# Optimization experiments

Hardware: AMD Instinct MI355X
Metric: run time of the kernel (lower is better)

## Reference

```python
import jax, jax.numpy as jnp
import numpy as np

D_MODEL = 1024
N_HEADS = 16
D_K = D_MODEL // N_HEADS
BATCH = 2
SEQ = 2048


def setup_inputs() -> dict:
    key = jax.random.key(0)
    ks = jax.random.split(key, 9)
    s = 1.0 / np.sqrt(D_MODEL)
    x = jax.random.normal(ks[0], (BATCH, SEQ, D_MODEL), dtype=jnp.float32)
    # nn.Linear params: weight [out, in], bias [out]
    w_q = jax.random.uniform(ks[1], (D_MODEL, D_MODEL), jnp.float32, -s, s)
    b_q = jax.random.uniform(ks[2], (D_MODEL,), jnp.float32, -s, s)
    w_k = jax.random.uniform(ks[3], (D_MODEL, D_MODEL), jnp.float32, -s, s)
    b_k = jax.random.uniform(ks[4], (D_MODEL,), jnp.float32, -s, s)
    w_v = jax.random.uniform(ks[5], (D_MODEL, D_MODEL), jnp.float32, -s, s)
    b_v = jax.random.uniform(ks[6], (D_MODEL,), jnp.float32, -s, s)
    w_o = jax.random.uniform(ks[7], (D_MODEL, D_MODEL), jnp.float32, -s, s)
    b_o = jax.random.uniform(ks[8], (D_MODEL,), jnp.float32, -s, s)
    return {"x": x, "w_q": w_q, "b_q": b_q, "w_k": w_k, "b_k": b_k,
            "w_v": w_v, "b_v": b_v, "w_o": w_o, "b_o": b_o}


def reference(x, w_q, b_q, w_k, b_k, w_v, b_v, w_o, b_o):
    B, S, _ = x.shape
    # Linear projections, then split heads: [B, H, S, d_k]
    def proj(w, b):
        y = jnp.einsum('bsd,ed->bse', x, w) + b
        return y.reshape(B, S, N_HEADS, D_K).transpose(0, 2, 1, 3)
    q = proj(w_q, b_q)
    k = proj(w_k, b_k)
    v = proj(w_v, b_v)
    scores = jnp.einsum('bhqd,bhkd->bhqk', q, k) / jnp.sqrt(jnp.float32(D_K))
    attn = jax.nn.softmax(scores, axis=-1)  # dropout is identity in eval mode
    out = jnp.einsum('bhqk,bhkd->bhqd', attn, v)
    out = out.transpose(0, 2, 1, 3).reshape(B, S, D_MODEL)
    out = jnp.einsum('bsd,ed->bse', out, w_o) + b_o
    return out, attn
```

## Files before the change

### kernel.cpp

```cpp
#include <hip/hip_runtime.h>
#include <hip/hip_bf16.h>
#include <stdint.h>


typedef __attribute__((ext_vector_type(4))) float f32x4;
typedef __attribute__((ext_vector_type(8))) short s16x8;
typedef __attribute__((ext_vector_type(4))) unsigned short u16x4;

#define MFMA(a, b, c) __builtin_amdgcn_mfma_f32_16x16x32_bf16((a), (b), (c), 0, 0, 0)

__device__ __forceinline__ unsigned short f2bf(float f) {
    unsigned int u = __float_as_uint(f);
    unsigned int r = (u + 0x7FFFu + ((u >> 16) & 1u)) >> 16;
    return (unsigned short)r;
}

__global__ void convert_kernel(const float* __restrict__ x,
                               const float* __restrict__ wq, const float* __restrict__ wk,
                               const float* __restrict__ wv, const float* __restrict__ wo,
                               unsigned short* __restrict__ xb, unsigned short* __restrict__ wb) {
    size_t g = (size_t)blockIdx.x * blockDim.x + threadIdx.x;
    size_t i4 = g * 4;
    const float* src;
    unsigned short* dst;
    size_t off;
    if (i4 < 4194304) {
        src = x; dst = xb; off = i4;
    } else {
        size_t j = i4 - 4194304;
        int wsel = (int)(j >> 20);
        off = j & 1048575;
        src = (wsel == 0) ? wq : (wsel == 1) ? wk : (wsel == 2) ? wv : wo;
        dst = wb + ((size_t)wsel << 20);
    }
    float4 v = *(const float4*)(src + off);
    u16x4 o;
    o[0] = f2bf(v.x); o[1] = f2bf(v.y); o[2] = f2bf(v.z); o[3] = f2bf(v.w);
    *(u16x4*)(dst + off) = o;
}

__global__ __launch_bounds__(256, 2) void gemm_kernel(
    const unsigned short* __restrict__ A, const unsigned short* __restrict__ B,
    const float* __restrict__ bias_q, const float* __restrict__ bias_k,
    const float* __restrict__ bias_v, int mode,
    unsigned short* __restrict__ Qs, unsigned short* __restrict__ Kb,
    unsigned short* __restrict__ Vt, float* __restrict__ outp) {
    const int t = threadIdx.x;
    const int lane = t & 63;
    const int w = t >> 6;
    const int wr = w >> 1, wc = w & 1;
    const int rowbase = blockIdx.y * 128;
    const int colbase = blockIdx.x * 128;

    __shared__ unsigned short lA[2][128 * 40];
    __shared__ unsigned short lB[2][128 * 40];

    const int sr = t >> 2;
    const int sc = (t & 3) * 8;

    const unsigned short* gA0 = A + (size_t)(rowbase + sr) * 1024 + sc;
    const unsigned short* gA1 = A + (size_t)(rowbase + sr + 64) * 1024 + sc;
    const unsigned short* gB0 = B + (size_t)(colbase + sr) * 1024 + sc;
    const unsigned short* gB1 = B + (size_t)(colbase + sr + 64) * 1024 + sc;

    f32x4 acc[4][4];
#pragma unroll
    for (int mi = 0; mi < 4; ++mi)
#pragma unroll
        for (int ni = 0; ni < 4; ++ni)
            acc[mi][ni] = (f32x4){0.f, 0.f, 0.f, 0.f};

    uint4 va0 = *(const uint4*)(gA0);
    uint4 va1 = *(const uint4*)(gA1);
    uint4 vb0 = *(const uint4*)(gB0);
    uint4 vb1 = *(const uint4*)(gB1);
    *(uint4*)&lA[0][sr * 40 + sc] = va0;
    *(uint4*)&lA[0][(sr + 64) * 40 + sc] = va1;
    *(uint4*)&lB[0][sr * 40 + sc] = vb0;
    *(uint4*)&lB[0][(sr + 64) * 40 + sc] = vb1;
    __syncthreads();

    const int koff = (lane >> 4) * 8;
    const int ar = wr * 64 + (lane & 15);
    const int br = wc * 64 + (lane & 15);

    int cur = 0;
    for (int kt = 0; kt < 32; ++kt) {
        if (kt < 31) {
            int ko = (kt + 1) * 32;
            va0 = *(const uint4*)(gA0 + ko);
            va1 = *(const uint4*)(gA1 + ko);
            vb0 = *(const uint4*)(gB0 + ko);
            vb1 = *(const uint4*)(gB1 + ko);
        }
        s16x8 af[4], bf[4];
#pragma unroll
        for (int mi = 0; mi < 4; ++mi)
            af[mi] = *(const s16x8*)&lA[cur][(ar + mi * 16) * 40 + koff];
#pragma unroll
        for (int ni = 0; ni < 4; ++ni)
            bf[ni] = *(const s16x8*)&lB[cur][(br + ni * 16) * 40 + koff];
#pragma unroll
        for (int mi = 0; mi < 4; ++mi)
#pragma unroll
            for (int ni = 0; ni < 4; ++ni)
                acc[mi][ni] = MFMA(af[mi], bf[ni], acc[mi][ni]);
        if (kt < 31) {
            int nb = cur ^ 1;
            *(uint4*)&lA[nb][sr * 40 + sc] = va0;
            *(uint4*)&lA[nb][(sr + 64) * 40 + sc] = va1;
            *(uint4*)&lB[nb][sr * 40 + sc] = vb0;
            *(uint4*)&lB[nb][(sr + 64) * 40 + sc] = vb1;
        }
        __syncthreads();
        cur ^= 1;
    }

    if (mode == 1) {
#pragma unroll
        for (int ni = 0; ni < 4; ++ni) {
            int n = colbase + wc * 64 + ni * 16 + (lane & 15);
            float bv = bias_q[n];
#pragma unroll
            for (int mi = 0; mi < 4; ++mi) {
#pragma unroll
                for (int reg = 0; reg < 4; ++reg) {
                    int m = rowbase + wr * 64 + mi * 16 + (lane >> 4) * 4 + reg;
                    outp[(size_t)m * 1024 + n] = acc[mi][ni][reg] + bv;
                }
            }
        }
    } else {
        const int proj = colbase >> 10;
        const float* bias = (proj == 0) ? bias_q : (proj == 1) ? bias_k : bias_v;
        const float scale = (proj == 0) ? 0.18033688011112042f : 1.0f;
#pragma unroll
        for (int ni = 0; ni < 4; ++ni) {
            int n = colbase + wc * 64 + ni * 16 + (lane & 15);
            int nn = n & 1023;
            int h = nn >> 6, d = nn & 63;
            float bv = bias[nn];
#pragma unroll
            for (int mi = 0; mi < 4; ++mi) {
                int m0 = rowbase + wr * 64 + mi * 16 + (lane >> 4) * 4;
                int b = m0 >> 11, s0 = m0 & 2047;
                if (proj == 2) {
                    u16x4 pk;
#pragma unroll
                    for (int reg = 0; reg < 4; ++reg)
                        pk[reg] = f2bf(acc[mi][ni][reg] + bv);
                    *(u16x4*)&Vt[((size_t)(b * 16 + h) * 64 + d) * 2048 + s0] = pk;
                } else {
                    unsigned short* dstp = (proj == 0) ? Qs : Kb;
#pragma unroll
                    for (int reg = 0; reg < 4; ++reg)
                        dstp[((size_t)(b * 16 + h) * 2048 + (s0 + reg)) * 64 + d] =
                            f2bf((acc[mi][ni][reg] + bv) * scale);
                }
            }
        }
    }
}

__global__ __launch_bounds__(256, 2) void attn_kernel(
    const unsigned short* __restrict__ Qs, const unsigned short* __restrict__ Kb,
    const unsigned short* __restrict__ Vt, float* __restrict__ attn,
    unsigned short* __restrict__ ctx) {
    const int t = threadIdx.x;
    const int lane = t & 63;
    const int w = t >> 6;
    const int wr = w >> 1, wc = w & 1;
    const int qt = blockIdx.x;
    const int bh = blockIdx.y;
    const int b = bh >> 4, h = bh & 15;

    const unsigned short* Qh = Qs + (size_t)bh * (2048 * 64);
    const unsigned short* Kh = Kb + (size_t)bh * (2048 * 64);
    const unsigned short* Vh = Vt + (size_t)bh * (64 * 2048);
    float* attn_h = attn + (size_t)bh * (2048 * 2048) + (size_t)qt * (128 * 2048);

    __shared__ unsigned short lQ[128 * 72];
    __shared__ unsigned short lK[64 * 72];
    __shared__ unsigned short lV[64 * 72];
    __shared__ unsigned short lP[128 * 72];
    __shared__ float lred[2][128];

    const int sr8 = t >> 3;
    const int sc8 = (t & 7) * 8;

    {
#pragma unroll
        for (int rr = 0; rr < 4; ++rr) {
            uint4 v = *(const uint4*)&Qh[((size_t)(qt * 128 + sr8 + rr * 32)) * 64 + sc8];
            *(uint4*)&lQ[(sr8 + rr * 32) * 72 + sc8] = v;
        }
    }

    const int koff = (lane >> 4) * 8;
    const int ar = wr * 64 + (lane & 15);
    const int brc = wc * 32 + (lane & 15);

    float lsum[4][4];
#pragma unroll
    for (int mi = 0; mi < 4; ++mi)
#pragma unroll
        for (int reg = 0; reg < 4; ++reg) lsum[mi][reg] = 0.f;

    for (int kt = 0; kt < 32; ++kt) {
        __syncthreads();
        uint4 kv0 = *(const uint4*)&Kh[((size_t)(kt * 64 + sr8)) * 64 + sc8];
        uint4 kv1 = *(const uint4*)&Kh[((size_t)(kt * 64 + sr8 + 32)) * 64 + sc8];
        *(uint4*)&lK[sr8 * 72 + sc8] = kv0;
        *(uint4*)&lK[(sr8 + 32) * 72 + sc8] = kv1;
        __syncthreads();
        f32x4 sacc[4][2];
#pragma unroll
        for (int mi = 0; mi < 4; ++mi)
#pragma unroll
            for (int ni = 0; ni < 2; ++ni) sacc[mi][ni] = (f32x4){0.f, 0.f, 0.f, 0.f};
#pragma unroll
        for (int kk = 0; kk < 2; ++kk) {
            s16x8 qf[4], kf[2];
#pragma unroll
            for (int mi = 0; mi < 4; ++mi)
                qf[mi] = *(const s16x8*)&lQ[(ar + mi * 16) * 72 + kk * 32 + koff];
#pragma unroll
            for (int ni = 0; ni < 2; ++ni)
                kf[ni] = *(const s16x8*)&lK[(brc + ni * 16) * 72 + kk * 32 + koff];
#pragma unroll
            for (int mi = 0; mi < 4; ++mi)
#pragma unroll
                for (int ni = 0; ni < 2; ++ni)
                    sacc[mi][ni] = MFMA(qf[mi], kf[ni], sacc[mi][ni]);
        }
#pragma unroll
        for (int mi = 0; mi < 4; ++mi) {
#pragma unroll
            for (int reg = 0; reg < 4; ++reg) {
                float e = exp2f(sacc[mi][0][reg]) + exp2f(sacc[mi][1][reg]);
                e += __shfl_xor(e, 1);
                e += __shfl_xor(e, 2);
                e += __shfl_xor(e, 4);
                e += __shfl_xor(e, 8);
                lsum[mi][reg] += e;
            }
        }
    }
    if ((lane & 15) == 0) {
#pragma unroll
        for (int mi = 0; mi < 4; ++mi)
#pragma unroll
            for (int reg = 0; reg < 4; ++reg)
                lred[wc][wr * 64 + mi * 16 + (lane >> 4) * 4 + reg] = lsum[mi][reg];
    }
    __syncthreads();
    float rl[4][4];
#pragma unroll
    for (int mi = 0; mi < 4; ++mi)
#pragma unroll
        for (int reg = 0; reg < 4; ++reg) {
            int row = wr * 64 + mi * 16 + (lane >> 4) * 4 + reg;
            rl[mi][reg] = 1.0f / (lred[0][row] + lred[1][row]);
        }

    f32x4 oacc[4][2];
#pragma unroll
    for (int mi = 0; mi < 4; ++mi)
#pragma unroll
        for (int ni = 0; ni < 2; ++ni) oacc[mi][ni] = (f32x4){0.f, 0.f, 0.f, 0.f};

    for (int kt = 0; kt < 32; ++kt) {
        __syncthreads();
        uint4 kv0 = *(const uint4*)&Kh[((size_t)(kt * 64 + sr8)) * 64 + sc8];
        uint4 kv1 = *(const uint4*)&Kh[((size_t)(kt * 64 + sr8 + 32)) * 64 + sc8];
        uint4 vv0 = *(const uint4*)&Vh[(size_t)sr8 * 2048 + kt * 64 + sc8];
        uint4 vv1 = *(const uint4*)&Vh[(size_t)(sr8 + 32) * 2048 + kt * 64 + sc8];
        *(uint4*)&lK[sr8 * 72 + sc8] = kv0;
        *(uint4*)&lK[(sr8 + 32) * 72 + sc8] = kv1;
        *(uint4*)&lV[sr8 * 72 + sc8] = vv0;
        *(uint4*)&lV[(sr8 + 32) * 72 + sc8] = vv1;
        __syncthreads();
        f32x4 sacc[4][2];
#pragma unroll
        for (int mi = 0; mi < 4; ++mi)
#pragma unroll
            for (int ni = 0; ni < 2; ++ni) sacc[mi][ni] = (f32x4){0.f, 0.f, 0.f, 0.f};
#pragma unroll
        for (int kk = 0; kk < 2; ++kk) {
            s16x8 qf[4], kf[2];
#pragma unroll
            for (int mi = 0; mi < 4; ++mi)
                qf[mi] = *(const s16x8*)&lQ[(ar + mi * 16) * 72 + kk * 32 + koff];
#pragma unroll
            for (int ni = 0; ni < 2; ++ni)
                kf[ni] = *(const s16x8*)&lK[(brc + ni * 16) * 72 + kk * 32 + koff];
#pragma unroll
            for (int mi = 0; mi < 4; ++mi)
#pragma unroll
                for (int ni = 0; ni < 2; ++ni)
                    sacc[mi][ni] = MFMA(qf[mi], kf[ni], sacc[mi][ni]);
        }
#pragma unroll
        for (int mi = 0; mi < 4; ++mi) {
#pragma unroll
            for (int ni = 0; ni < 2; ++ni) {
                int coll = wc * 32 + ni * 16 + (lane & 15);
                int colg = kt * 64 + coll;
#pragma unroll
                for (int reg = 0; reg < 4; ++reg) {
                    int row = wr * 64 + mi * 16 + (lane >> 4) * 4 + reg;
                    float p = exp2f(sacc[mi][ni][reg]) * rl[mi][reg];
                    attn_h[(size_t)row * 2048 + colg] = p;
                    lP[row * 72 + coll] = f2bf(p);
                }
            }
        }
        __syncthreads();
#pragma unroll
        for (int ks = 0; ks < 2; ++ks) {
            s16x8 pf[4], vf[2];
#pragma unroll
            for (int mi = 0; mi < 4; ++mi)
                pf[mi] = *(const s16x8*)&lP[(ar + mi * 16) * 72 + ks * 32 + koff];
#pragma unroll
            for (int ni = 0; ni < 2; ++ni)
                vf[ni] = *(const s16x8*)&lV[(brc + ni * 16) * 72 + ks * 32 + koff];
#pragma unroll
            for (int mi = 0; mi < 4; ++mi)
#pragma unroll
                for (int ni = 0; ni < 2; ++ni)
                    oacc[mi][ni] = MFMA(pf[mi], vf[ni], oacc[mi][ni]);
        }
    }

#pragma unroll
    for (int mi = 0; mi < 4; ++mi) {
#pragma unroll
        for (int ni = 0; ni < 2; ++ni) {
            int d = wc * 32 + ni * 16 + (lane & 15);
#pragma unroll
            for (int reg = 0; reg < 4; ++reg) {
                int q = qt * 128 + wr * 64 + mi * 16 + (lane >> 4) * 4 + reg;
                ctx[((size_t)(b * 2048 + q)) * 1024 + h * 64 + d] = f2bf(oacc[mi][ni][reg]);
            }
        }
    }
}

extern "C" void kernel_launch(void* const* d_in, const int* in_sizes, int n_in,
                              void* d_out, int out_size, void* d_ws, size_t ws_size,
                              hipStream_t stream) {
    const float* x  = (const float*)d_in[0];
    const float* wq = (const float*)d_in[1];
    const float* bq = (const float*)d_in[2];
    const float* wk = (const float*)d_in[3];
    const float* bk = (const float*)d_in[4];
    const float* wv = (const float*)d_in[5];
    const float* bv = (const float*)d_in[6];
    const float* wo = (const float*)d_in[7];
    const float* bo = (const float*)d_in[8];

    char* ws = (char*)d_ws;
    unsigned short* xb  = (unsigned short*)(ws);
    unsigned short* wb  = (unsigned short*)(ws + 8388608);
    unsigned short* Qsc = (unsigned short*)(ws + 16777216);
    unsigned short* Kb  = (unsigned short*)(ws + 25165824);
    unsigned short* Vt  = (unsigned short*)(ws + 33554432);
    unsigned short* ctx = (unsigned short*)(ws + 41943040);

    float* out  = (float*)d_out;
    float* attn = out + 4194304;

    convert_kernel<<<8192, 256, 0, stream>>>(x, wq, wk, wv, wo, xb, wb);
    gemm_kernel<<<dim3(24, 32), 256, 0, stream>>>(xb, wb, bq, bk, bv, 0,
                                                  Qsc, Kb, Vt, nullptr);
    attn_kernel<<<dim3(16, 32), 256, 0, stream>>>(Qsc, Kb, Vt, attn, ctx);
    gemm_kernel<<<dim3(8, 32), 256, 0, stream>>>(ctx, wb + 3 * 1048576, bo, bo, bo, 1,
                                                 nullptr, nullptr, nullptr, out);
}
```

Baseline: 312.4 us.

## Load attention Q/K/V fragments directly into registers and prefetch next tile

After: 277.4 us. 1.13x faster.

```diff
diff --git a/kernel.cpp b/kernel.cpp
--- a/kernel.cpp
+++ b/kernel.cpp
@@ -168,6 +168,9 @@
     unsigned short* __restrict__ ctx) {
     const int t = threadIdx.x;
     const int lane = t & 63;
+    const int l15 = lane & 15;
+    const int g = lane >> 4;
+    const int g4 = g * 4, g8 = g * 8;
     const int w = t >> 6;
     const int wr = w >> 1, wc = w & 1;
     const int qt = blockIdx.x;
@@ -177,174 +180,157 @@
     const unsigned short* Qh = Qs + (size_t)bh * (2048 * 64);
     const unsigned short* Kh = Kb + (size_t)bh * (2048 * 64);
     const unsigned short* Vh = Vt + (size_t)bh * (64 * 2048);
-    float* attn_h = attn + (size_t)bh * (2048 * 2048) + (size_t)qt * (128 * 2048);
-
-    __shared__ unsigned short lQ[128 * 72];
-    __shared__ unsigned short lK[64 * 72];
-    __shared__ unsigned short lV[64 * 72];
-    __shared__ unsigned short lP[128 * 72];
+    float* attn_h = attn + (size_t)bh * (2048 * 2048) + (size_t)(qt * 128) * 2048;
+
+    __shared__ unsigned short lP[2][128 * 72];
     __shared__ float lred[2][128];
 
-    const int sr8 = t >> 3;
-    const int sc8 = (t & 7) * 8;
-
-    {
-#pragma unroll
-        for (int rr = 0; rr < 4; ++rr) {
-            uint4 v = *(const uint4*)&Qh[((size_t)(qt * 128 + sr8 + rr * 32)) * 64 + sc8];
-            *(uint4*)&lQ[(sr8 + rr * 32) * 72 + sc8] = v;
-        }
-    }
-
-    const int koff = (lane >> 4) * 8;
-    const int ar = wr * 64 + (lane & 15);
-    const int brc = wc * 32 + (lane & 15);
-
-    float lsum[4][4];
+    s16x8 qf[8];
 #pragma unroll
     for (int mi = 0; mi < 4; ++mi)
 #pragma unroll
-        for (int reg = 0; reg < 4; ++reg) lsum[mi][reg] = 0.f;
-
-    for (int kt = 0; kt < 32; ++kt) {
-        __syncthreads();
-        uint4 kv0 = *(const uint4*)&Kh[((size_t)(kt * 64 + sr8)) * 64 + sc8];
-        uint4 kv1 = *(const uint4*)&Kh[((size_t)(kt * 64 + sr8 + 32)) * 64 + sc8];
-        *(uint4*)&lK[sr8 * 72 + sc8] = kv0;
-        *(uint4*)&lK[(sr8 + 32) * 72 + sc8] = kv1;
-        __syncthreads();
-        f32x4 sacc[4][2];
+        for (int kk = 0; kk < 2; ++kk)
+            qf[mi * 2 + kk] =
+                *(const s16x8*)&Qh[(size_t)(qt * 128 + wr * 64 + mi * 16 + l15) * 64 + kk * 32 + g8];
+
+    s16x8 kf0[4], kf1[4], vf0[4], vf1[4];
+
+#define K_LOAD(DST, KT)                                                                     \
+    {                                                                                       \
+        _Pragma("unroll") for (int ni = 0; ni < 2; ++ni)                                    \
+            _Pragma("unroll") for (int kk = 0; kk < 2; ++kk)                                \
+                DST[ni * 2 + kk] = *(const s16x8*)&Kh[(size_t)((KT) * 64 + wc * 32 +        \
+                                                               ni * 16 + l15) * 64 +        \
+                                                      kk * 32 + g8];                        \
+    }
+#define V_LOAD(DST, KT)                                                                     \
+    {                                                                                       \
+        _Pragma("unroll") for (int ni = 0; ni < 2; ++ni)                                    \
+            _Pragma("unroll") for (int ks = 0; ks < 2; ++ks)                                \
+                DST[ni * 2 + ks] = *(const s16x8*)&Vh[(size_t)(wc * 32 + ni * 16 + l15) *   \
+                                                          2048 +                            \
+                                                      (KT) * 64 + ks * 32 + g8];            \
+    }
+#define QK_MFMA(KF, SACC)                                                                   \
+    {                                                                                       \
+        _Pragma("unroll") for (int kk = 0; kk < 2; ++kk)                                    \
+            _Pragma("unroll") for (int mi = 0; mi < 4; ++mi)                                \
+                _Pragma("unroll") for (int ni = 0; ni < 2; ++ni)                            \
+                    SACC[mi][ni] = MFMA(KF[ni * 2 + kk], qf[mi * 2 + kk], SACC[mi][ni]);    \
+    }
+
+    float qsum[4] = {0.f, 0.f, 0.f, 0.f};
+    K_LOAD(kf0, 0);
+#define P1_BODY(KF, KFN, KT)                                                                \
+    {                                                                                       \
+        f32x4 sacc[4][2];                                                                   \
+        _Pragma("unroll") for (int mi = 0; mi < 4; ++mi)                                    \
+            _Pragma("unroll") for (int ni = 0; ni < 2; ++ni)                                \
+                sacc[mi][ni] = (f32x4){0.f, 0.f, 0.f, 0.f};                                 \
+        QK_MFMA(KF, sacc);                                                                  \
+        if ((KT) < 31) K_LOAD(KFN, (KT) + 1);                                               \
+        _Pragma("unroll") for (int mi = 0; mi < 4; ++mi) {                                  \
+            float e = 0.f;                                                                  \
+            _Pragma("unroll") for (int ni = 0; ni < 2; ++ni)                                \
+                _Pragma("unroll") for (int r = 0; r < 4; ++r)                               \
+                    e += exp2f(sacc[mi][ni][r]);                                            \
+            qsum[mi] += e;                                                                  \
+        }                                                                                   \
+    }
+    for (int k2 = 0; k2 < 16; ++k2) {
+        P1_BODY(kf0, kf1, 2 * k2);
+        P1_BODY(kf1, kf0, 2 * k2 + 1);
+    }
+#pragma unroll
+    for (int mi = 0; mi < 4; ++mi) {
+        float v = qsum[mi];
+        v += __shfl_xor(v, 16);
+        v += __shfl_xor(v, 32);
+        qsum[mi] = v;
+    }
+    if (lane < 16) {
 #pragma unroll
         for (int mi = 0; mi < 4; ++mi)
-#pragma unroll
-            for (int ni = 0; ni < 2; ++ni) sacc[mi][ni] = (f32x4){0.f, 0.f, 0.f, 0.f};
-#pragma unroll
-        for (int kk = 0; kk < 2; ++kk) {
-            s16x8 qf[4], kf[2];
-#pragma unroll
-            for (int mi = 0; mi < 4; ++mi)
-                qf[mi] = *(const s16x8*)&lQ[(ar + mi * 16) * 72 + kk * 32 + koff];
-#pragma unroll
-            for (int ni = 0; ni < 2; ++ni)
-                kf[ni] = *(const s16x8*)&lK[(brc + ni * 16) * 72 + kk * 32 + koff];
-#pragma unroll
-            for (int mi = 0; mi < 4; ++mi)
-#pragma unroll
-                for (int ni = 0; ni < 2; ++ni)
-                    sacc[mi][ni] = MFMA(qf[mi], kf[ni], sacc[mi][ni]);
-        }
-#pragma unroll
-        for (int mi = 0; mi < 4; ++mi) {
-#pragma unroll
-            for (int reg = 0; reg < 4; ++reg) {
-                float e = exp2f(sacc[mi][0][reg]) + exp2f(sacc[mi][1][reg]);
-                e += __shfl_xor(e, 1);
-                e += __shfl_xor(e, 2);
-                e += __shfl_xor(e, 4);
-                e += __shfl_xor(e, 8);
-                lsum[mi][reg] += e;
+            lred[wc][wr * 64 + mi * 16 + lane] = qsum[mi];
+    }
+    __syncthreads();
+    float rl[4];
+#pragma unroll
+    for (int mi = 0; mi < 4; ++mi) {
+        int q = wr * 64 + mi * 16 + l15;
+        rl[mi] = 1.0f / (lred[0][q] + lred[1][q]);
+    }
+
+    f32x4 oacc[4][2];
+#pragma unroll
+    for (int mi = 0; mi < 4; ++mi)
+#pragma unroll
+        for (int ni = 0; ni < 2; ++ni) oacc[mi][ni] = (f32x4){0.f, 0.f, 0.f, 0.f};
+
+    K_LOAD(kf0, 0);
+    V_LOAD(vf0, 0);
+#define P2_BODY(BUF, KF, KFN, VF, VFN, KT)                                                  \
+    {                                                                                       \
+        f32x4 sacc[4][2];                                                                   \
+        _Pragma("unroll") for (int mi = 0; mi < 4; ++mi)                                    \
+            _Pragma("unroll") for (int ni = 0; ni < 2; ++ni)                                \
+                sacc[mi][ni] = (f32x4){0.f, 0.f, 0.f, 0.f};                                 \
+        QK_MFMA(KF, sacc);                                                                  \
+        if ((KT) < 31) {                                                                    \
+            K_LOAD(KFN, (KT) + 1);                                                          \
+            V_LOAD(VFN, (KT) + 1);                                                          \
+        }                                                                                   \
+        _Pragma("unroll") for (int mi = 0; mi < 4; ++mi) {                                  \
+            const int q = wr * 64 + mi * 16 + l15;                                          \
+            _Pragma("unroll") for (int ni = 0; ni < 2; ++ni) {                              \
+                float4 pv;                                                                  \
+                pv.x = exp2f(sacc[mi][ni][0]) * rl[mi];                                     \
+                pv.y = exp2f(sacc[mi][ni][1]) * rl[mi];                                     \
+                pv.z = exp2f(sacc[mi][ni][2]) * rl[mi];                                     \
+                pv.w = exp2f(sacc[mi][ni][3]) * rl[mi];                                     \
+                *(float4*)&attn_h[(size_t)q * 2048 + (KT) * 64 + wc * 32 + ni * 16 + g4] =  \
+                    pv;                                                                     \
+                u16x4 pk;                                                                   \
+                pk[0] = f2bf(pv.x);                                                         \
+                pk[1] = f2bf(pv.y);                                                         \
+                pk[2] = f2bf(pv.z);                                                         \
+                pk[3] = f2bf(pv.w);                                                         \
+                *(u16x4*)&lP[BUF][q * 72 + wc * 32 + ni * 16 + g4] = pk;                    \
+            }                                                                               \
+        }                                                                                   \
+        __syncthreads();                                                                    \
+        _Pragma("unroll") for (int ks = 0; ks < 2; ++ks) {                                  \
+            s16x8 pf[4];                                                                    \
+            _Pragma("unroll") for (int mi = 0; mi < 4; ++mi)                                \
+                pf[mi] =                                                                    \
+                    *(const s16x8*)&lP[BUF][(wr * 64 + mi * 16 + l15) * 72 + ks * 32 + g8]; \
+            _Pragma("unroll") for (int mi = 0; mi < 4; ++mi)                                \
+                _Pragma("unroll") for (int ni = 0; ni < 2; ++ni)                            \
+                    oacc[mi][ni] = MFMA(pf[mi], VF[ni * 2 + ks], oacc[mi][ni]);             \
+        }                                                                                   \
+    }
+    for (int k2 = 0; k2 < 16; ++k2) {
+        P2_BODY(0, kf0, kf1, vf0, vf1, 2 * k2);
+        P2_BODY(1, kf1, kf0, vf1, vf0, 2 * k2 + 1);
+    }
+
+#pragma unroll
+    for (int mi = 0; mi < 4; ++mi) {
+#pragma unroll
+        for (int ni = 0; ni < 2; ++ni) {
+            int d = wc * 32 + ni * 16 + l15;
+#pragma unroll
+            for (int r = 0; r < 4; ++r) {
+                int q = qt * 128 + wr * 64 + mi * 16 + g4 + r;
+                ctx[((size_t)(b * 2048 + q)) * 1024 + h * 64 + d] = f2bf(oacc[mi][ni][r]);
             }
         }
     }
-    if ((lane & 15) == 0) {
-#pragma unroll
-        for (int mi = 0; mi < 4; ++mi)
-#pragma unroll
-            for (int reg = 0; reg < 4; ++reg)
-                lred[wc][wr * 64 + mi * 16 + (lane >> 4) * 4 + reg] = lsum[mi][reg];
-    }
-    __syncthreads();
-    float rl[4][4];
-#pragma unroll
-    for (int mi = 0; mi < 4; ++mi)
-#pragma unroll
-        for (int reg = 0; reg < 4; ++reg) {
-            int row = wr * 64 + mi * 16 + (lane >> 4) * 4 + reg;
-            rl[mi][reg] = 1.0f / (lred[0][row] + lred[1][row]);
-        }
-
-    f32x4 oacc[4][2];
-#pragma unroll
-    for (int mi = 0; mi < 4; ++mi)
-#pragma unroll
-        for (int ni = 0; ni < 2; ++ni) oacc[mi][ni] = (f32x4){0.f, 0.f, 0.f, 0.f};
-
-    for (int kt = 0; kt < 32; ++kt) {
-        __syncthreads();
-        uint4 kv0 = *(const uint4*)&Kh[((size_t)(kt * 64 + sr8)) * 64 + sc8];
-        uint4 kv1 = *(const uint4*)&Kh[((size_t)(kt * 64 + sr8 + 32)) * 64 + sc8];
-        uint4 vv0 = *(const uint4*)&Vh[(size_t)sr8 * 2048 + kt * 64 + sc8];
-        uint4 vv1 = *(const uint4*)&Vh[(size_t)(sr8 + 32) * 2048 + kt * 64 + sc8];
-        *(uint4*)&lK[sr8 * 72 + sc8] = kv0;
-        *(uint4*)&lK[(sr8 + 32) * 72 + sc8] = kv1;
-        *(uint4*)&lV[sr8 * 72 + sc8] = vv0;
-        *(uint4*)&lV[(sr8 + 32) * 72 + sc8] = vv1;
-        __syncthreads();
-        f32x4 sacc[4][2];
-#pragma unroll
-        for (int mi = 0; mi < 4; ++mi)
-#pragma unroll
-            for (int ni = 0; ni < 2; ++ni) sacc[mi][ni] = (f32x4){0.f, 0.f, 0.f, 0.f};
-#pragma unroll
-        for (int kk = 0; kk < 2; ++kk) {
-            s16x8 qf[4], kf[2];
-#pragma unroll
-            for (int mi = 0; mi < 4; ++mi)
-                qf[mi] = *(const s16x8*)&lQ[(ar + mi * 16) * 72 + kk * 32 + koff];
-#pragma unroll
-            for (int ni = 0; ni < 2; ++ni)
-                kf[ni] = *(const s16x8*)&lK[(brc + ni * 16) * 72 + kk * 32 + koff];
-#pragma unroll
-            for (int mi = 0; mi < 4; ++mi)
-#pragma unroll
-                for (int ni = 0; ni < 2; ++ni)
-                    sacc[mi][ni] = MFMA(qf[mi], kf[ni], sacc[mi][ni]);
-        }
-#pragma unroll
-        for (int mi = 0; mi < 4; ++mi) {
-#pragma unroll
-            for (int ni = 0; ni < 2; ++ni) {
-                int coll = wc * 32 + ni * 16 + (lane & 15);
-                int colg = kt * 64 + coll;
-#pragma unroll
-                for (int reg = 0; reg < 4; ++reg) {
-                    int row = wr * 64 + mi * 16 + (lane >> 4) * 4 + reg;
-                    float p = exp2f(sacc[mi][ni][reg]) * rl[mi][reg];
-                    attn_h[(size_t)row * 2048 + colg] = p;
-                    lP[row * 72 + coll] = f2bf(p);
-                }
-            }
-        }
-        __syncthreads();
-#pragma unroll
-        for (int ks = 0; ks < 2; ++ks) {
-            s16x8 pf[4], vf[2];
-#pragma unroll
-            for (int mi = 0; mi < 4; ++mi)
-                pf[mi] = *(const s16x8*)&lP[(ar + mi * 16) * 72 + ks * 32 + koff];
-#pragma unroll
-            for (int ni = 0; ni < 2; ++ni)
-                vf[ni] = *(const s16x8*)&lV[(brc + ni * 16) * 72 + ks * 32 + koff];
-#pragma unroll
-            for (int mi = 0; mi < 4; ++mi)
-#pragma unroll
-                for (int ni = 0; ni < 2; ++ni)
-                    oacc[mi][ni] = MFMA(pf[mi], vf[ni], oacc[mi][ni]);
-        }
-    }
-
-#pragma unroll
-    for (int mi = 0; mi < 4; ++mi) {
-#pragma unroll
-        for (int ni = 0; ni < 2; ++ni) {
-            int d = wc * 32 + ni * 16 + (lane & 15);
-#pragma unroll
-            for (int reg = 0; reg < 4; ++reg) {
-                int q = qt * 128 + wr * 64 + mi * 16 + (lane >> 4) * 4 + reg;
-                ctx[((size_t)(b * 2048 + q)) * 1024 + h * 64 + d] = f2bf(oacc[mi][ni][reg]);
-            }
-        }
-    }
+#undef K_LOAD
+#undef V_LOAD
+#undef QK_MFMA
+#undef P1_BODY
+#undef P2_BODY
 }
 
 extern "C" void kernel_launch(void* const* d_in, const int* in_sizes, int n_in,
```
